# Kernel optimization log

Hardware: AMD Instinct MI355X
Metric: run time of the kernel (lower is better)

Reference implementation:

```python
import jax, jax.numpy as jnp
import numpy as np

C = 512
GROUPS = 32
EPS = 1e-6


def group_norm(x, w, b):
    # x: [B, C, H, W]
    B, Cc, H, W = x.shape
    xg = x.reshape(B, GROUPS, Cc // GROUPS, H, W)
    mean = xg.mean(axis=(2, 3, 4), keepdims=True)
    var = xg.var(axis=(2, 3, 4), keepdims=True)
    xn = (xg - mean) * jax.lax.rsqrt(var + EPS)
    xn = xn.reshape(B, Cc, H, W)
    return xn * w[None, :, None, None] + b[None, :, None, None]


def conv1x1(x, w, b):
    # 1x1 conv == per-pixel linear: w [Cout, Cin], x [B, Cin, H, W]
    return jnp.einsum('oc,bchw->bohw', w, x) + b[None, :, None, None]


def setup_inputs() -> dict:
    key = jax.random.key(0)
    ks = jax.random.split(key, 11)
    B, H, W = 4, 64, 64
    s = 1.0 / np.sqrt(C)
    return {
        'x': jax.random.normal(ks[0], (B, C, H, W), dtype=jnp.float32),
        'gn_w': jnp.ones((C,), dtype=jnp.float32),
        'gn_b': jnp.zeros((C,), dtype=jnp.float32),
        'wq': jax.random.normal(ks[1], (C, C), dtype=jnp.float32) * s,
        'bq': jnp.zeros((C,), dtype=jnp.float32),
        'wk': jax.random.normal(ks[2], (C, C), dtype=jnp.float32) * s,
        'bk': jnp.zeros((C,), dtype=jnp.float32),
        'wv': jax.random.normal(ks[3], (C, C), dtype=jnp.float32) * s,
        'bv': jnp.zeros((C,), dtype=jnp.float32),
        'wo': jax.random.normal(ks[4], (C, C), dtype=jnp.float32) * s,
        'bo': jnp.zeros((C,), dtype=jnp.float32),
    }


def reference(x, gn_w, gn_b, wq, bq, wk, bk, wv, bv, wo, bo):
    B, Cc, H, W = x.shape
    scale = Cc ** (-0.5)
    xn = group_norm(x, gn_w, gn_b)
    q = conv1x1(xn, wq, bq).reshape(B, Cc, H * W)
    k = conv1x1(xn, wk, bk).reshape(B, Cc, H * W)
    v = conv1x1(xn, wv, bv).reshape(B, Cc, H * W)
    attn = jax.nn.softmax(jnp.einsum('bci,bcj->bij', q, k) * scale, axis=2)
    out = jnp.einsum('bij,bcj->bci', attn, v).reshape(B, Cc, H, W)
    out = conv1x1(out, wo, bo)
    return x + out
```

## Files before the change

### kernel.cpp

```cpp
#include <hip/hip_runtime.h>

#define NB 4
#define CC 512
#define NSP 4096
#define NGRP 32

using bf16x8 = __attribute__((ext_vector_type(8))) __bf16;
using f32x4  = __attribute__((ext_vector_type(4))) float;

__device__ __forceinline__ unsigned short f2bf(float f) {
  union { float f; unsigned int u; } v; v.f = f;
  unsigned int r = v.u + 0x7fffu + ((v.u >> 16) & 1u);
  return (unsigned short)(r >> 16);
}
__device__ __forceinline__ float bf2f(unsigned short h) {
  union { unsigned int u; float f; } v; v.u = ((unsigned int)h) << 16;
  return v.f;
}

__global__ __launch_bounds__(256) void cvt_w_kernel(const float* __restrict__ wq,
    const float* __restrict__ wk, const float* __restrict__ wv,
    const float* __restrict__ wo, unsigned short* __restrict__ out) {
  int i = blockIdx.x * 256 + threadIdx.x;
  out[i]          = f2bf(wq[i]);
  out[i + 262144] = f2bf(wk[i]);
  out[i + 524288] = f2bf(wv[i]);
  out[i + 786432] = f2bf(wo[i]);
}

__global__ __launch_bounds__(256) void gn_stats_kernel(const float* __restrict__ x,
                                                       float* __restrict__ stats) {
  const int b = blockIdx.x >> 5, g = blockIdx.x & 31;
  const float4* p = reinterpret_cast<const float4*>(x + ((size_t)b * CC + g * 16) * NSP);
  float s = 0.f, ss = 0.f;
  for (int i = threadIdx.x; i < 16384; i += 256) {
    float4 v = p[i];
    s  += v.x + v.y + v.z + v.w;
    ss += v.x * v.x + v.y * v.y + v.z * v.z + v.w * v.w;
  }
  __shared__ float rs[4], rss[4];
  #pragma unroll
  for (int o = 32; o >= 1; o >>= 1) { s += __shfl_down(s, o); ss += __shfl_down(ss, o); }
  if ((threadIdx.x & 63) == 0) { rs[threadIdx.x >> 6] = s; rss[threadIdx.x >> 6] = ss; }
  __syncthreads();
  if (threadIdx.x == 0) {
    s = rs[0] + rs[1] + rs[2] + rs[3];
    ss = rss[0] + rss[1] + rss[2] + rss[3];
    float mean = s * (1.f / 65536.f);
    float var = ss * (1.f / 65536.f) - mean * mean;
    stats[blockIdx.x * 2 + 0] = mean;
    stats[blockIdx.x * 2 + 1] = rsqrtf(var + 1e-6f);
  }
}

__global__ __launch_bounds__(256) void gn_apply_kernel(const float* __restrict__ x,
    const float* __restrict__ stats, const float* __restrict__ gw,
    const float* __restrict__ gb, unsigned short* __restrict__ xnT) {
  const int b = blockIdx.z, c0 = blockIdx.y * 32, n0 = blockIdx.x * 32;
  __shared__ unsigned short tile[32][33];
  const int tx = threadIdx.x & 31, ty = threadIdx.x >> 5;
  #pragma unroll
  for (int r = 0; r < 4; ++r) {
    const int cl = ty + r * 8;
    const int c = c0 + cl;
    const int g = c >> 4;
    const float mean = stats[(b * 32 + g) * 2];
    const float rstd = stats[(b * 32 + g) * 2 + 1];
    const float sc = rstd * gw[c];
    const float sh = gb[c] - mean * sc;
    const float v = x[((size_t)b * CC + c) * NSP + n0 + tx];
    tile[cl][tx] = f2bf(v * sc + sh);
  }
  __syncthreads();
  #pragma unroll
  for (int r = 0; r < 4; ++r) {
    const int nl = ty + r * 8;
    xnT[((size_t)b * NSP + n0 + nl) * CC + c0 + tx] = tile[tx][nl];
  }
}

__global__ __launch_bounds__(256) void sum_reduce_kernel(const float* __restrict__ part,
                                                         float* __restrict__ invl) {
  const int row = blockIdx.x * 4 + (threadIdx.x >> 6);
  const int lane = threadIdx.x & 63;
  float v = part[((size_t)row << 6) + lane];
  #pragma unroll
  for (int msk = 1; msk <= 32; msk <<= 1) v += __shfl_xor(v, msk);
  if (lane == 0) invl[row] = 1.f / v;
}

template<int BIAS, bool OBF16, bool RESID>
__global__ __launch_bounds__(256) void gemm2(
    const unsigned short* __restrict__ A, const unsigned short* __restrict__ B,
    const float* __restrict__ bias, const float* __restrict__ resid,
    void* __restrict__ Cout, int M, int N, int K, float scale,
    long long sAb, long long sBb, long long sCb, long long sRb) {
  __shared__ __align__(16) unsigned short sA[2][128 * 64];
  __shared__ __align__(16) unsigned short sB[2][128 * 64];
  const int tid = threadIdx.x;
  const int lane = tid & 63;
  const int wid  = tid >> 6;

  const unsigned nwg = gridDim.x * gridDim.y * gridDim.z;
  unsigned lin = blockIdx.x + gridDim.x * (blockIdx.y + gridDim.y * blockIdx.z);
  lin = (lin & 7) * (nwg >> 3) + (lin >> 3);
  const int bn = lin % gridDim.x;
  const unsigned t2 = lin / gridDim.x;
  const int bm = t2 % gridDim.y;
  const int b  = t2 / gridDim.y;

  const unsigned short* Ab = A + (size_t)b * sAb + (size_t)bm * 128 * K;
  const unsigned short* Bb = B + (size_t)b * sBb + (size_t)bn * 128 * K;
  const int wm = wid >> 1, wn = wid & 1;
  const int l15 = lane & 15, h = lane >> 4;

  f32x4 acc[4][4] = {};

  auto stage = [&](int buf, int k0) {
    #pragma unroll
    for (int it = 0; it < 4; ++it) {
      const int o  = (it * 256 + tid) * 16;
      const int r  = o >> 7;
      const int c2 = (o & 127) ^ ((r & 7) << 4);
      __builtin_amdgcn_global_load_lds(
          (const __attribute__((address_space(1))) void*)((const char*)(Ab + (size_t)r * K + k0) + c2),
          (__attribute__((address_space(3))) void*)((char*)sA[buf] + o), 16, 0, 0);
      __builtin_amdgcn_global_load_lds(
          (const __attribute__((address_space(1))) void*)((const char*)(Bb + (size_t)r * K + k0) + c2),
          (__attribute__((address_space(3))) void*)((char*)sB[buf] + o), 16, 0, 0);
    }
  };

  int abase[4], bbase[4];
  #pragma unroll
  for (int i = 0; i < 4; ++i) {
    const int ar = wm * 64 + i * 16 + l15;
    abase[i] = ar * 128 + (((ar & 7) << 4) ^ (h << 4));
    const int br = wn * 64 + i * 16 + l15;
    bbase[i] = br * 128 + (((br & 7) << 4) ^ (h << 4));
  }

  stage(0, 0);
  const int NT = K >> 6;
  #pragma unroll 1
  for (int t = 0; t < NT; ++t) {
    const int cur = t & 1;
    if (t + 1 < NT) {
      stage(cur ^ 1, (t + 1) << 6);
      asm volatile("s_waitcnt vmcnt(8)" ::: "memory");
    } else {
      asm volatile("s_waitcnt vmcnt(0)" ::: "memory");
    }
    __builtin_amdgcn_sched_barrier(0);
    __builtin_amdgcn_s_barrier();
    __builtin_amdgcn_sched_barrier(0);

    const char* cA = (const char*)sA[cur];
    const char* cB = (const char*)sB[cur];
    #pragma unroll
    for (int kk = 0; kk < 2; ++kk) {
      bf16x8 af[4], bfr[4];
      #pragma unroll
      for (int m = 0; m < 4; ++m)
        af[m] = *reinterpret_cast<const bf16x8*>(cA + (abase[m] ^ (kk << 6)));
      #pragma unroll
      for (int n = 0; n < 4; ++n)
        bfr[n] = *reinterpret_cast<const bf16x8*>(cB + (bbase[n] ^ (kk << 6)));
      #pragma unroll
      for (int m = 0; m < 4; ++m)
        #pragma unroll
        for (int n = 0; n < 4; ++n)
          acc[m][n] = __builtin_amdgcn_mfma_f32_16x16x32_bf16(af[m], bfr[n], acc[m][n], 0, 0, 0);
    }
    __builtin_amdgcn_sched_barrier(0);
    __builtin_amdgcn_s_barrier();
    __builtin_amdgcn_sched_barrier(0);
  }

  float* outf = (float*)Cout;
  unsigned short* outh = (unsigned short*)Cout;
  const size_t cb = (size_t)b * sCb;
  #pragma unroll
  for (int m = 0; m < 4; ++m) {
    #pragma unroll
    for (int r = 0; r < 4; ++r) {
      const int row = bm * 128 + wm * 64 + m * 16 + h * 4 + r;
      #pragma unroll
      for (int n = 0; n < 4; ++n) {
        const int col = bn * 128 + wn * 64 + n * 16 + l15;
        float vv = acc[m][n][r];
        if constexpr (BIAS == 1) vv += bias[row];
        if constexpr (BIAS == 2) vv += bias[col];
        vv *= scale;
        if constexpr (RESID) vv += resid[(size_t)b * sRb + (size_t)row * N + col];
        const size_t oi = cb + (size_t)row * N + col;
        if constexpr (OBF16) outh[oi] = f2bf(vv);
        else outf[oi] = vv;
      }
    }
  }
}

template<int BM, int BN, int WMS, int WNS, bool EXPOUT, bool INVL>
__global__ __launch_bounds__(512) void gemm8(
    const unsigned short* __restrict__ A, const unsigned short* __restrict__ B,
    void* __restrict__ Cout, const float* __restrict__ invl_in,
    float* __restrict__ part_out, int N, int K, float scale,
    long long sAb, long long sBb, long long sCb) {
  constexpr int WR = BM / WMS;
  constexpr int M_REP = WR / 16;
  constexpr int LOADS = BM / 64 + BN / 64;
  __shared__ __align__(16) unsigned short sA[2][BM * 64];
  __shared__ __align__(16) unsigned short sB[2][BN * 64];
  const int tid = threadIdx.x;
  const int lane = tid & 63;
  const int wid  = tid >> 6;

  const unsigned nwg = gridDim.x * gridDim.y * gridDim.z;
  unsigned lin = blockIdx.x + gridDim.x * (blockIdx.y + gridDim.y * blockIdx.z);
  lin = (lin & 7) * (nwg >> 3) + (lin >> 3);
  const int bn = lin % gridDim.x;
  const unsigned t2 = lin / gridDim.x;
  const int bm = t2 % gridDim.y;
  const int b  = t2 / gridDim.y;

  const unsigned short* Ab = A + (size_t)b * sAb + (size_t)bm * BM * K;
  const unsigned short* Bb = B + (size_t)b * sBb + (size_t)bn * BN * K;
  const int wm = wid / WNS, wn = wid % WNS;
  const int l15 = lane & 15, h = lane >> 4;

  f32x4 acc[M_REP][4] = {};

  auto stage = [&](int buf, int k0) {
    #pragma unroll
    for (int it = 0; it < BM / 64; ++it) {
      const int o  = (it * 512 + tid) * 16;
      const int r  = o >> 7;
      const int c2 = (o & 127) ^ ((r & 7) << 4);
      __builtin_amdgcn_global_load_lds(
          (const __attribute__((address_space(1))) void*)((const char*)(Ab + (size_t)r * K + k0) + c2),
          (__attribute__((address_space(3))) void*)((char*)sA[buf] + o), 16, 0, 0);
    }
    #pragma unroll
    for (int it = 0; it < BN / 64; ++it) {
      const int o  = (it * 512 + tid) * 16;
      const int r  = o >> 7;
      const int c2 = (o & 127) ^ ((r & 7) << 4);
      __builtin_amdgcn_global_load_lds(
          (const __attribute__((address_space(1))) void*)((const char*)(Bb + (size_t)r * K + k0) + c2),
          (__attribute__((address_space(3))) void*)((char*)sB[buf] + o), 16, 0, 0);
    }
  };

  int abase[M_REP], bbase[4];
  #pragma unroll
  for (int i = 0; i < M_REP; ++i) {
    const int ar = wm * WR + i * 16 + l15;
    abase[i] = ar * 128 + (((ar & 7) << 4) ^ (h << 4));
  }
  #pragma unroll
  for (int i = 0; i < 4; ++i) {
    const int br = wn * 64 + i * 16 + l15;
    bbase[i] = br * 128 + (((br & 7) << 4) ^ (h << 4));
  }

  stage(0, 0);
  const int NT = K >> 6;
  #pragma unroll 1
  for (int t = 0; t < NT; ++t) {
    const int cur = t & 1;
    if (t + 1 < NT) {
      stage(cur ^ 1, (t + 1) << 6);
      if constexpr (LOADS == 8) asm volatile("s_waitcnt vmcnt(8)" ::: "memory");
      else                      asm volatile("s_waitcnt vmcnt(6)" ::: "memory");
    } else {
      asm volatile("s_waitcnt vmcnt(0)" ::: "memory");
    }
    __builtin_amdgcn_sched_barrier(0);
    __builtin_amdgcn_s_barrier();
    __builtin_amdgcn_sched_barrier(0);

    const char* cA = (const char*)sA[cur];
    const char* cB = (const char*)sB[cur];

    bf16x8 bfr[2][4];
    #pragma unroll
    for (int kk = 0; kk < 2; ++kk)
      #pragma unroll
      for (int n = 0; n < 4; ++n)
        bfr[kk][n] = *reinterpret_cast<const bf16x8*>(cB + (bbase[n] ^ (kk << 6)));

    #pragma unroll
    for (int p = 0; p < M_REP / 2; ++p) {
      bf16x8 af[2][2];
      #pragma unroll
      for (int i = 0; i < 2; ++i)
        #pragma unroll
        for (int kk = 0; kk < 2; ++kk)
          af[kk][i] = *reinterpret_cast<const bf16x8*>(cA + (abase[2 * p + i] ^ (kk << 6)));
      asm volatile("s_waitcnt lgkmcnt(0)" ::: "memory");
      __builtin_amdgcn_sched_barrier(0);
      __builtin_amdgcn_s_setprio(1);
      #pragma unroll
      for (int i = 0; i < 2; ++i)
        #pragma unroll
        for (int n = 0; n < 4; ++n)
          #pragma unroll
          for (int kk = 0; kk < 2; ++kk)
            acc[2 * p + i][n] =
                __builtin_amdgcn_mfma_f32_16x16x32_bf16(af[kk][i], bfr[kk][n], acc[2 * p + i][n], 0, 0, 0);
      __builtin_amdgcn_s_setprio(0);
      __builtin_amdgcn_sched_barrier(0);
      __builtin_amdgcn_s_barrier();
      __builtin_amdgcn_sched_barrier(0);
    }
  }

  unsigned short* outh = (unsigned short*)Cout;
  const size_t cb = (size_t)b * sCb;
  #pragma unroll
  for (int m = 0; m < M_REP; ++m) {
    #pragma unroll
    for (int r = 0; r < 4; ++r) {
      const int row = bm * BM + wm * WR + m * 16 + h * 4 + r;
      if constexpr (EXPOUT) {
        float se = 0.f;
        #pragma unroll
        for (int n = 0; n < 4; ++n) {
          const int col = bn * BN + wn * 64 + n * 16 + l15;
          unsigned short pb = f2bf(__expf(fminf(acc[m][n][r] * scale, 80.f)));
          outh[cb + (size_t)row * N + col] = pb;
          se += bf2f(pb);
        }
        #pragma unroll
        for (int msk = 1; msk <= 8; msk <<= 1) se += __shfl_xor(se, msk);
        if (l15 == 0)
          part_out[(((size_t)b * NSP + row) << 6) + bn * (BN / 64) + wn] = se;
      } else {
        float invl = 1.0f;
        if constexpr (INVL) invl = invl_in[(size_t)b * NSP + row];
        #pragma unroll
        for (int n = 0; n < 4; ++n) {
          const int col = bn * BN + wn * 64 + n * 16 + l15;
          outh[cb + (size_t)row * N + col] = f2bf(acc[m][n][r] * scale * invl);
        }
      }
    }
  }
}

extern "C" void kernel_launch(void* const* d_in, const int* in_sizes, int n_in,
                              void* d_out, int out_size, void* d_ws, size_t ws_size,
                              hipStream_t stream) {
  const float* x    = (const float*)d_in[0];
  const float* gn_w = (const float*)d_in[1];
  const float* gn_b = (const float*)d_in[2];
  const float* wq   = (const float*)d_in[3];
  const float* bq   = (const float*)d_in[4];
  const float* wk   = (const float*)d_in[5];
  const float* bk   = (const float*)d_in[6];
  const float* wv   = (const float*)d_in[7];
  const float* bv   = (const float*)d_in[8];
  const float* wo   = (const float*)d_in[9];
  const float* bo   = (const float*)d_in[10];
  float* out = (float*)d_out;

  char* ws = (char*)d_ws;
  const size_t NC = (size_t)NSP * CC;
  unsigned short* wq_bf = (unsigned short*)ws;
  unsigned short* wk_bf = wq_bf + 262144;
  unsigned short* wv_bf = wq_bf + 524288;
  unsigned short* wo_bf = wq_bf + 786432;
  unsigned short* xnT   = wq_bf + 1048576;
  unsigned short* qT    = xnT + NB * NC;
  unsigned short* kT    = qT + NB * NC;
  unsigned short* vC    = kT + NB * NC;
  unsigned short* aoutT = vC + NB * NC;
  float* gstats = (float*)(aoutT + NB * NC);
  unsigned short* S = (unsigned short*)((char*)gstats + 1024);
  float* part = (float*)(S + (size_t)NB * NSP * NSP);
  float* invl = part + ((size_t)NB * NSP << 6);

  const float scale = 0.04419417382415922f;
  const size_t SS = (size_t)NSP * NSP;

  cvt_w_kernel<<<1024, 256, 0, stream>>>(wq, wk, wv, wo, wq_bf);
  gn_stats_kernel<<<NB * NGRP, 256, 0, stream>>>(x, gstats);
  gn_apply_kernel<<<dim3(NSP / 32, CC / 32, NB), 256, 0, stream>>>(x, gstats, gn_w, gn_b, xnT);

  gemm2<2, true, false><<<dim3(CC / 128, NSP / 128, NB), 256, 0, stream>>>(
      xnT, wq_bf, bq, nullptr, qT, NSP, CC, CC, scale, NC, 0, NC, 0);
  gemm2<2, true, false><<<dim3(CC / 128, NSP / 128, NB), 256, 0, stream>>>(
      xnT, wk_bf, bk, nullptr, kT, NSP, CC, CC, 1.0f, NC, 0, NC, 0);
  gemm2<1, true, false><<<dim3(NSP / 128, CC / 128, NB), 256, 0, stream>>>(
      wv_bf, xnT, bv, nullptr, vC, CC, NSP, CC, 1.0f, 0, NC, NC, 0);

  gemm8<256, 256, 2, 4, true, false><<<dim3(NSP / 256, NSP / 256, NB), 512, 0, stream>>>(
      qT, kT, S, nullptr, part, NSP, CC, 1.0f, NC, NC, (long long)SS);
  sum_reduce_kernel<<<NB * NSP / 4, 256, 0, stream>>>(part, invl);
  gemm8<256, 128, 4, 2, false, true><<<dim3(CC / 128, NSP / 256, NB), 512, 0, stream>>>(
      S, vC, aoutT, invl, nullptr, CC, NSP, 1.0f, SS, NC, NC);

  gemm2<1, false, true><<<dim3(NSP / 128, CC / 128, NB), 256, 0, stream>>>(
      wo_bf, aoutT, bo, x, out, CC, NSP, CC, 1.0f, 0, NC, NC, NC);
}
```

Measured before the change: 305.5 us.

## Specialize attention GEMMs to 256x128 tiles with triple-buffered LDS prefetch

Replaces the templated gemm8 with a fixed 256x128-tile gemm3 that keeps three LDS stages in flight, prefetching two K-tiles ahead instead of one. It also drops the per-pair inner barrier and setprio, loads all A/B fragments once per K-step, then issues all MFMAs. The QK^T GEMM now uses 256x128 tiles instead of 256x256, so its grid doubles. The goal is to hide global-to-LDS latency and cut barrier overhead. In exchange LDS use rises to 144KB per block, which limits occupancy, and QK^T loses some operand reuse.

```diff
diff --git a/kernel.cpp b/kernel.cpp
--- a/kernel.cpp
+++ b/kernel.cpp
@@ -201,17 +201,14 @@
   }
 }
 
-template<int BM, int BN, int WMS, int WNS, bool EXPOUT, bool INVL>
-__global__ __launch_bounds__(512) void gemm8(
+template<bool EXPOUT, bool INVL>
+__global__ __launch_bounds__(512) void gemm3(
     const unsigned short* __restrict__ A, const unsigned short* __restrict__ B,
     void* __restrict__ Cout, const float* __restrict__ invl_in,
     float* __restrict__ part_out, int N, int K, float scale,
     long long sAb, long long sBb, long long sCb) {
-  constexpr int WR = BM / WMS;
-  constexpr int M_REP = WR / 16;
-  constexpr int LOADS = BM / 64 + BN / 64;
-  __shared__ __align__(16) unsigned short sA[2][BM * 64];
-  __shared__ __align__(16) unsigned short sB[2][BN * 64];
+  __shared__ __align__(16) unsigned short sA[3][256 * 64];
+  __shared__ __align__(16) unsigned short sB[3][128 * 64];
   const int tid = threadIdx.x;
   const int lane = tid & 63;
   const int wid  = tid >> 6;
@@ -224,16 +221,16 @@
   const int bm = t2 % gridDim.y;
   const int b  = t2 / gridDim.y;
 
-  const unsigned short* Ab = A + (size_t)b * sAb + (size_t)bm * BM * K;
-  const unsigned short* Bb = B + (size_t)b * sBb + (size_t)bn * BN * K;
-  const int wm = wid / WNS, wn = wid % WNS;
+  const unsigned short* Ab = A + (size_t)b * sAb + (size_t)bm * 256 * K;
+  const unsigned short* Bb = B + (size_t)b * sBb + (size_t)bn * 128 * K;
+  const int wm = wid >> 1, wn = wid & 1;
   const int l15 = lane & 15, h = lane >> 4;
 
-  f32x4 acc[M_REP][4] = {};
+  f32x4 acc[4][4] = {};
 
   auto stage = [&](int buf, int k0) {
     #pragma unroll
-    for (int it = 0; it < BM / 64; ++it) {
+    for (int it = 0; it < 4; ++it) {
       const int o  = (it * 512 + tid) * 16;
       const int r  = o >> 7;
       const int c2 = (o & 127) ^ ((r & 7) << 4);
@@ -242,7 +239,7 @@
           (__attribute__((address_space(3))) void*)((char*)sA[buf] + o), 16, 0, 0);
     }
     #pragma unroll
-    for (int it = 0; it < BN / 64; ++it) {
+    for (int it = 0; it < 2; ++it) {
       const int o  = (it * 512 + tid) * 16;
       const int r  = o >> 7;
       const int c2 = (o & 127) ^ ((r & 7) << 4);
@@ -252,27 +249,27 @@
     }
   };
 
-  int abase[M_REP], bbase[4];
-  #pragma unroll
-  for (int i = 0; i < M_REP; ++i) {
-    const int ar = wm * WR + i * 16 + l15;
+  int abase[4], bbase[4];
+  #pragma unroll
+  for (int i = 0; i < 4; ++i) {
+    const int ar = wm * 64 + i * 16 + l15;
     abase[i] = ar * 128 + (((ar & 7) << 4) ^ (h << 4));
-  }
-  #pragma unroll
-  for (int i = 0; i < 4; ++i) {
     const int br = wn * 64 + i * 16 + l15;
     bbase[i] = br * 128 + (((br & 7) << 4) ^ (h << 4));
   }
 
+  const int NT = K >> 6;
   stage(0, 0);
-  const int NT = K >> 6;
+  stage(1, 64);
+  int cur = 0;
   #pragma unroll 1
   for (int t = 0; t < NT; ++t) {
-    const int cur = t & 1;
-    if (t + 1 < NT) {
-      stage(cur ^ 1, (t + 1) << 6);
-      if constexpr (LOADS == 8) asm volatile("s_waitcnt vmcnt(8)" ::: "memory");
-      else                      asm volatile("s_waitcnt vmcnt(6)" ::: "memory");
+    if (t + 2 < NT) {
+      int nb = cur + 2; if (nb >= 3) nb -= 3;
+      stage(nb, (t + 2) << 6);
+      asm volatile("s_waitcnt vmcnt(12)" ::: "memory");
+    } else if (t + 1 < NT) {
+      asm volatile("s_waitcnt vmcnt(6)" ::: "memory");
     } else {
       asm volatile("s_waitcnt vmcnt(0)" ::: "memory");
     }
@@ -282,52 +279,41 @@
 
     const char* cA = (const char*)sA[cur];
     const char* cB = (const char*)sB[cur];
-
-    bf16x8 bfr[2][4];
-    #pragma unroll
-    for (int kk = 0; kk < 2; ++kk)
+    bf16x8 af[2][4], bfr[2][4];
+    #pragma unroll
+    for (int kk = 0; kk < 2; ++kk) {
+      #pragma unroll
+      for (int m = 0; m < 4; ++m)
+        af[kk][m] = *reinterpret_cast<const bf16x8*>(cA + (abase[m] ^ (kk << 6)));
       #pragma unroll
       for (int n = 0; n < 4; ++n)
         bfr[kk][n] = *reinterpret_cast<const bf16x8*>(cB + (bbase[n] ^ (kk << 6)));
-
-    #pragma unroll
-    for (int p = 0; p < M_REP / 2; ++p) {
-      bf16x8 af[2][2];
-      #pragma unroll
-      for (int i = 0; i < 2; ++i)
-        #pragma unroll
-        for (int kk = 0; kk < 2; ++kk)
-          af[kk][i] = *reinterpret_cast<const bf16x8*>(cA + (abase[2 * p + i] ^ (kk << 6)));
-      asm volatile("s_waitcnt lgkmcnt(0)" ::: "memory");
-      __builtin_amdgcn_sched_barrier(0);
-      __builtin_amdgcn_s_setprio(1);
-      #pragma unroll
-      for (int i = 0; i < 2; ++i)
+    }
+    #pragma unroll
+    for (int kk = 0; kk < 2; ++kk)
+      #pragma unroll
+      for (int m = 0; m < 4; ++m)
         #pragma unroll
         for (int n = 0; n < 4; ++n)
-          #pragma unroll
-          for (int kk = 0; kk < 2; ++kk)
-            acc[2 * p + i][n] =
-                __builtin_amdgcn_mfma_f32_16x16x32_bf16(af[kk][i], bfr[kk][n], acc[2 * p + i][n], 0, 0, 0);
-      __builtin_amdgcn_s_setprio(0);
-      __builtin_amdgcn_sched_barrier(0);
-      __builtin_amdgcn_s_barrier();
-      __builtin_amdgcn_sched_barrier(0);
-    }
+          acc[m][n] = __builtin_amdgcn_mfma_f32_16x16x32_bf16(af[kk][m], bfr[kk][n], acc[m][n], 0, 0, 0);
+    __builtin_amdgcn_sched_barrier(0);
+    __builtin_amdgcn_s_barrier();
+    __builtin_amdgcn_sched_barrier(0);
+    ++cur; if (cur >= 3) cur = 0;
   }
 
   unsigned short* outh = (unsigned short*)Cout;
   const size_t cb = (size_t)b * sCb;
   #pragma unroll
-  for (int m = 0; m < M_REP; ++m) {
+  for (int m = 0; m < 4; ++m) {
     #pragma unroll
     for (int r = 0; r < 4; ++r) {
-      const int row = bm * BM + wm * WR + m * 16 + h * 4 + r;
+      const int row = bm * 256 + wm * 64 + m * 16 + h * 4 + r;
       if constexpr (EXPOUT) {
         float se = 0.f;
         #pragma unroll
         for (int n = 0; n < 4; ++n) {
-          const int col = bn * BN + wn * 64 + n * 16 + l15;
+          const int col = bn * 128 + wn * 64 + n * 16 + l15;
           unsigned short pb = f2bf(__expf(fminf(acc[m][n][r] * scale, 80.f)));
           outh[cb + (size_t)row * N + col] = pb;
           se += bf2f(pb);
@@ -335,13 +321,13 @@
         #pragma unroll
         for (int msk = 1; msk <= 8; msk <<= 1) se += __shfl_xor(se, msk);
         if (l15 == 0)
-          part_out[(((size_t)b * NSP + row) << 6) + bn * (BN / 64) + wn] = se;
+          part_out[(((size_t)b * NSP + row) << 6) + bn * 2 + wn] = se;
       } else {
         float invl = 1.0f;
         if constexpr (INVL) invl = invl_in[(size_t)b * NSP + row];
         #pragma unroll
         for (int n = 0; n < 4; ++n) {
-          const int col = bn * BN + wn * 64 + n * 16 + l15;
+          const int col = bn * 128 + wn * 64 + n * 16 + l15;
           outh[cb + (size_t)row * N + col] = f2bf(acc[m][n][r] * scale * invl);
         }
       }
@@ -395,10 +381,10 @@
   gemm2<1, true, false><<<dim3(NSP / 128, CC / 128, NB), 256, 0, stream>>>(
       wv_bf, xnT, bv, nullptr, vC, CC, NSP, CC, 1.0f, 0, NC, NC, 0);
 
-  gemm8<256, 256, 2, 4, true, false><<<dim3(NSP / 256, NSP / 256, NB), 512, 0, stream>>>(
+  gemm3<true, false><<<dim3(NSP / 128, NSP / 256, NB), 512, 0, stream>>>(
       qT, kT, S, nullptr, part, NSP, CC, 1.0f, NC, NC, (long long)SS);
   sum_reduce_kernel<<<NB * NSP / 4, 256, 0, stream>>>(part, invl);
-  gemm8<256, 128, 4, 2, false, true><<<dim3(CC / 128, NSP / 256, NB), 512, 0, stream>>>(
+  gemm3<false, true><<<dim3(CC / 128, NSP / 256, NB), 512, 0, stream>>>(
       S, vC, aoutT, invl, nullptr, CC, NSP, 1.0f, SS, NC, NC);
 
   gemm2<1, false, true><<<dim3(NSP / 128, CC / 128, NB), 256, 0, stream>>>(
```

Result: slower. 324.0 us (+6.1%).
